# Performance work log

Hardware: AMD Instinct MI355X
Metric: run time of the kernel (lower is better)

Reference implementation:

```python
import jax, jax.numpy as jnp
import numpy as np

B, S, E, H = 2, 2048, 1024, 16
D = E // H  # head_dim = 64

def setup_inputs() -> dict:
    key = jax.random.key(0)
    ks = jax.random.split(key, 11)
    s = 1.0 / np.sqrt(E)
    inp = {
        'query': jax.random.normal(ks[0], (B, S, E), jnp.float32),
        'key':   jax.random.normal(ks[1], (B, S, E), jnp.float32),
        'value': jax.random.normal(ks[2], (B, S, E), jnp.float32),
        'Wq': jax.random.uniform(ks[3], (E, E), jnp.float32, -s, s),
        'bq': jax.random.uniform(ks[4], (E,), jnp.float32, -s, s),
        'Wk': jax.random.uniform(ks[5], (E, E), jnp.float32, -s, s),
        'bk': jax.random.uniform(ks[6], (E,), jnp.float32, -s, s),
        'Wv': jax.random.uniform(ks[7], (E, E), jnp.float32, -s, s),
        'bv': jax.random.uniform(ks[8], (E,), jnp.float32, -s, s),
        'Wo': jax.random.uniform(ks[9], (E, E), jnp.float32, -s, s),
        'bo': jax.random.uniform(ks[10], (E,), jnp.float32, -s, s),
    }
    return inp

def reference(query, key, value, Wq, bq, Wk, bk, Wv, bv, Wo, bo):
    # project and split heads: [B,S,E] -> [B,H,S,D]
    def proj(x, W, b):
        y = jnp.einsum('bse,fe->bsf', x, W) + b  # torch Linear: x @ W.T + b
        return y.reshape(B, S, H, D).transpose(0, 2, 1, 3)
    q = proj(query, Wq, bq)
    k = proj(key, Wk, bk)
    v = proj(value, Wv, bv)
    scores = jnp.einsum('bhqd,bhkd->bhqk', q, k) / jnp.sqrt(jnp.float32(D))
    attn = jax.nn.softmax(scores, axis=-1)
    out = jnp.einsum('bhqk,bhkd->bhqd', attn, v)  # [B,H,S,D]
    out = out.transpose(0, 2, 1, 3).reshape(B, S, E)
    return jnp.einsum('bse,fe->bsf', out, Wo) + bo
```

## Files before the change

### kernel.cpp

```cpp
#include <hip/hip_runtime.h>

#define B_ 2
#define S_ 2048
#define E_ 1024
#define H_ 16
#define D_ 64
#define M_ (B_*S_)
#define K_ E_

typedef __attribute__((ext_vector_type(8))) short  short8;
typedef __attribute__((ext_vector_type(4))) float  f32x4;
typedef __attribute__((ext_vector_type(8))) unsigned short u16x8;
typedef __attribute__((ext_vector_type(4))) unsigned short u16x4;
typedef __attribute__((ext_vector_type(4))) unsigned int   u32x4;

#define QSCALE 0.18033688011112042f

#if __has_builtin(__builtin_amdgcn_exp2f)
#define EXP2F(x) __builtin_amdgcn_exp2f(x)
#else
#define EXP2F(x) exp2f(x)
#endif

__device__ __forceinline__ unsigned short f2bf(float f) {
    unsigned u = __float_as_uint(f);
    u += 0x7fffu + ((u >> 16) & 1u);
    return (unsigned short)(u >> 16);
}

__device__ __forceinline__ void gl_lds16(const ushort* g, ushort* l) {
    __builtin_amdgcn_global_load_lds((const __attribute__((address_space(1))) void*)g,
                                     (__attribute__((address_space(3))) void*)l,
                                     16, 0, 0);
}

#define FL_SYNC(N) do {                                                   \
    asm volatile("s_waitcnt vmcnt(" #N ")" ::: "memory");                 \
    __builtin_amdgcn_s_barrier();                                         \
    asm volatile("" ::: "memory");                                        \
} while (0)

#define WAITL0_BAR() do {                                                 \
    asm volatile("s_waitcnt lgkmcnt(0)" ::: "memory");                    \
    __builtin_amdgcn_s_barrier();                                         \
    asm volatile("" ::: "memory");                                        \
} while (0)

__global__ __launch_bounds__(256)
void cvt_all(const float* __restrict__ q, const float* __restrict__ k,
             const float* __restrict__ v, const float* __restrict__ wq,
             const float* __restrict__ wk, const float* __restrict__ wv,
             const float* __restrict__ wo, ushort* __restrict__ dst)
{
    const int bid = blockIdx.x;
    const float* src;
    size_t dof;
    int local;
    if (bid < 6144) {
        const int t = bid >> 11;
        src = (t == 0) ? q : (t == 1) ? k : v;
        dof = (size_t)t * 4194304u;
        local = bid & 2047;
    } else {
        const int r = bid - 6144;
        const int t = r >> 9;
        src = (t == 0) ? wq : (t == 1) ? wk : (t == 2) ? wv : wo;
        dof = 12582912u + (size_t)t * 1048576u;
        local = r & 511;
    }
    const size_t idx = (size_t)local * 2048 + threadIdx.x * 8;
    const float4 a = *(const float4*)(src + idx);
    const float4 b = *(const float4*)(src + idx + 4);
    u16x8 o;
    o[0] = f2bf(a.x); o[1] = f2bf(a.y); o[2] = f2bf(a.z); o[3] = f2bf(a.w);
    o[4] = f2bf(b.x); o[5] = f2bf(b.y); o[6] = f2bf(b.z); o[7] = f2bf(b.w);
    *(u16x8*)(dst + dof + idx) = o;
}

template<int SWAP>
__device__ __forceinline__ void qkv_core(const ushort* __restrict__ X,
                                         const ushort* __restrict__ W,
                                         int m0, int n0,
                                         f32x4 acc[8][4], ushort* sh)
{
    const int tid  = threadIdx.x;
    const int lane = tid & 63;
    const int w    = tid >> 6;
    const int wm   = w & 1;
    const int wn   = w >> 1;
    const int l15  = lane & 15, quad = lane >> 4;

    const int srow = lane >> 3, schunk = lane & 7;
    const int scol = (schunk ^ srow) * 8;
    const ushort* pa[4]; const ushort* pb[4]; int loff[4];
    #pragma unroll
    for (int i = 0; i < 4; ++i) {
        const int row = (w * 4 + i) * 8 + srow;
        pa[i] = X + (size_t)(m0 + row) * K_ + scol;
        pb[i] = W + (size_t)(n0 + row) * K_ + scol;
        loff[i] = (w * 4 + i) * 512 + lane * 8;
    }

    const f32x4 zero = {0.f, 0.f, 0.f, 0.f};
    #pragma unroll
    for (int mt = 0; mt < 8; ++mt)
        #pragma unroll
        for (int nt = 0; nt < 4; ++nt) acc[mt][nt] = zero;

    #pragma unroll
    for (int i = 0; i < 4; ++i) {
        gl_lds16(pa[i],      sh + loff[i]);
        gl_lds16(pb[i],      sh + 16384 + loff[i]);
    }
    #pragma unroll
    for (int i = 0; i < 4; ++i) {
        gl_lds16(pa[i] + 64, sh + 32768 + loff[i]);
        gl_lds16(pb[i] + 64, sh + 32768 + 16384 + loff[i]);
    }

    const int arow = wm * 128 + l15;
    const int brow = wn * 64 + l15;

    for (int t = 0; t < 16; ++t) {
        ushort* curA = sh + (t & 1) * 32768;
        ushort* curB = curA + 16384;

        if (t < 15) { FL_SYNC(8); } else { FL_SYNC(0); }

        __builtin_amdgcn_s_setprio(1);
        #pragma unroll
        for (int kc = 0; kc < 2; ++kc) {
            short8 bf[4];
            #pragma unroll
            for (int nt = 0; nt < 4; ++nt) {
                const int r = brow + nt * 16;
                bf[nt] = *(const short8*)(curB + r * 64 + (((kc * 4 + quad) ^ (r & 7)) * 8));
            }
            #pragma unroll
            for (int mt = 0; mt < 8; ++mt) {
                const int r = arow + mt * 16;
                const short8 af = *(const short8*)(curA + r * 64 + (((kc * 4 + quad) ^ (r & 7)) * 8));
                #pragma unroll
                for (int nt = 0; nt < 4; ++nt) {
                    if (SWAP)
                        acc[mt][nt] = __builtin_amdgcn_mfma_f32_16x16x32_bf16(bf[nt], af, acc[mt][nt], 0, 0, 0);
                    else
                        acc[mt][nt] = __builtin_amdgcn_mfma_f32_16x16x32_bf16(af, bf[nt], acc[mt][nt], 0, 0, 0);
                }
            }
        }
        __builtin_amdgcn_s_setprio(0);

        if (t + 2 < 16) {
            WAITL0_BAR();
            const int k0 = (t + 2) * 64;
            #pragma unroll
            for (int i = 0; i < 4; ++i) {
                gl_lds16(pa[i] + k0, curA + loff[i]);
                gl_lds16(pb[i] + k0, curB + loff[i]);
            }
        }
    }
}

__global__ __launch_bounds__(512, 2)
void gemm_qkv(const ushort* __restrict__ Xq, const ushort* __restrict__ Xk,
              const ushort* __restrict__ Xv, const ushort* __restrict__ Wq,
              const ushort* __restrict__ Wk, const ushort* __restrict__ Wv,
              const float* __restrict__ bq, const float* __restrict__ bk,
              const float* __restrict__ bv, ushort* __restrict__ Qh,
              ushort* __restrict__ Kh, ushort* __restrict__ Vt)
{
    __shared__ ushort sh[65536];
    const int z = blockIdx.z;
    const ushort* X = (z == 0) ? Xq : (z == 1) ? Xk : Xv;
    const ushort* W = (z == 0) ? Wq : (z == 1) ? Wk : Wv;
    const float* bias = (z == 0) ? bq : (z == 1) ? bk : bv;
    ushort* dst = (z == 0) ? Qh : (z == 1) ? Kh : Vt;

    const int m0 = blockIdx.y * 256, n0 = blockIdx.x * 256;
    f32x4 acc[8][4];
    const int lane = threadIdx.x & 63, w = threadIdx.x >> 6;
    const int wm = w & 1, wn = w >> 1;
    const int l15 = lane & 15, quad = lane >> 4;

    if (z < 2) {
        qkv_core<1>(X, W, m0, n0, acc, sh);
        const float qsc = (z == 0) ? QSCALE : 1.0f;
        #pragma unroll
        for (int nt = 0; nt < 4; ++nt) {
            const int nb = n0 + wn * 64 + nt * 16 + quad * 4;
            const int h = nb >> 6, d0 = nb & 63;
            const float4 b4 = *(const float4*)(bias + nb);
            const float bb4[4] = {b4.x, b4.y, b4.z, b4.w};
            #pragma unroll
            for (int mt = 0; mt < 8; ++mt) {
                const int tok = m0 + wm * 128 + mt * 16 + l15;
                const int b = tok >> 11, s = tok & (S_ - 1);
                u16x4 pk;
                #pragma unroll
                for (int r = 0; r < 4; ++r)
                    pk[r] = f2bf((acc[mt][nt][r] + bb4[r]) * qsc);
                *(u16x4*)&dst[(((size_t)(b * H_ + h) * S_) + s) * D_ + d0] = pk;
            }
        }
    } else {
        qkv_core<0>(X, W, m0, n0, acc, sh);
        float bias4[4];
        #pragma unroll
        for (int nt = 0; nt < 4; ++nt)
            bias4[nt] = bias[n0 + wn * 64 + nt * 16 + l15];
        #pragma unroll
        for (int mt = 0; mt < 8; ++mt) {
            const int mrow0 = m0 + wm * 128 + mt * 16 + (quad * 4);
            const int b = mrow0 >> 11;
            const int s0 = mrow0 & (S_ - 1);
            #pragma unroll
            for (int nt = 0; nt < 4; ++nt) {
                const int n = n0 + wn * 64 + nt * 16 + l15;
                const int h = n >> 6, d = n & 63;
                u16x4 pk;
                #pragma unroll
                for (int r = 0; r < 4; ++r) pk[r] = f2bf(acc[mt][nt][r] + bias4[nt]);
                *(u16x4*)&Vt[(((size_t)(b * H_ + h) * D_) + d) * S_ + s0] = pk;
            }
        }
    }
}

__global__ __launch_bounds__(256)
void gemm_out(const ushort* __restrict__ X, const ushort* __restrict__ W,
              const float* __restrict__ bias, float* __restrict__ out)
{
    __shared__ ushort Ast[128 * 32];
    __shared__ ushort Bst[64 * 32];
    const int m0 = blockIdx.y * 128, n0 = blockIdx.x * 64;
    const int tid = threadIdx.x, lane = tid & 63, w = tid >> 6;
    const int wm = w & 1, wn = w >> 1;
    const int l15 = lane & 15, quad = lane >> 4;
    const int r0 = tid >> 2, c8 = (tid & 3) * 8;
    const int kb = quad * 8;

    const f32x4 zero = {0.f, 0.f, 0.f, 0.f};
    f32x4 acc[4][2];
    #pragma unroll
    for (int mt = 0; mt < 4; ++mt)
        #pragma unroll
        for (int nt = 0; nt < 2; ++nt) acc[mt][nt] = zero;

    for (int k0 = 0; k0 < K_; k0 += 32) {
        __syncthreads();
        const ushort* ga = X + (size_t)(m0 + r0) * K_ + k0 + c8;
        gl_lds16(ga, Ast + tid * 8);
        gl_lds16(ga + (size_t)64 * K_, Ast + 2048 + tid * 8);
        const ushort* gb = W + (size_t)(n0 + r0) * K_ + k0 + c8;
        gl_lds16(gb, Bst + tid * 8);
        __syncthreads();

        short8 af[4], bf[2];
        #pragma unroll
        for (int mt = 0; mt < 4; ++mt)
            af[mt] = *(const short8*)(Ast + (wm * 64 + mt * 16 + l15) * 32 + kb);
        #pragma unroll
        for (int nt = 0; nt < 2; ++nt)
            bf[nt] = *(const short8*)(Bst + (wn * 32 + nt * 16 + l15) * 32 + kb);
        #pragma unroll
        for (int mt = 0; mt < 4; ++mt)
            #pragma unroll
            for (int nt = 0; nt < 2; ++nt)
                acc[mt][nt] = __builtin_amdgcn_mfma_f32_16x16x32_bf16(af[mt], bf[nt], acc[mt][nt], 0, 0, 0);
    }

    float bias2[2];
    #pragma unroll
    for (int nt = 0; nt < 2; ++nt)
        bias2[nt] = bias[n0 + wn * 32 + nt * 16 + l15];

    #pragma unroll
    for (int mt = 0; mt < 4; ++mt) {
        const int mrow0 = m0 + wm * 64 + mt * 16 + quad * 4;
        #pragma unroll
        for (int nt = 0; nt < 2; ++nt) {
            const int n = n0 + wn * 32 + nt * 16 + l15;
            #pragma unroll
            for (int r = 0; r < 4; ++r)
                out[(size_t)(mrow0 + r) * E_ + n] = acc[mt][nt][r] + bias2[nt];
        }
    }
}

#define NTILE (S_ / 64)
#define QBLK 128

__device__ __forceinline__ void flash_stage(const ushort* __restrict__ Kg,
                                            const ushort* __restrict__ Vg,
                                            size_t qk_off, size_t vt_off,
                                            ushort* sh, int j,
                                            int row0, int gcol0, int row1, int gcol1,
                                            int chunk0, int chunk1, int lane)
{
    ushort* sb = sh + 8192 + (j & 1) * 8192;
    const int j0n = j * 64;
    gl_lds16(Kg + qk_off + (size_t)(j0n + row0) * D_ + gcol0 * 8, sb + chunk0 * 512 + lane * 8);
    gl_lds16(Vg + vt_off + (size_t)row0 * S_ + j0n + gcol0 * 8, sb + 4096 + chunk0 * 512 + lane * 8);
    gl_lds16(Kg + qk_off + (size_t)(j0n + row1) * D_ + gcol1 * 8, sb + chunk1 * 512 + lane * 8);
    gl_lds16(Vg + vt_off + (size_t)row1 * S_ + j0n + gcol1 * 8, sb + 4096 + chunk1 * 512 + lane * 8);
}

__global__ __launch_bounds__(256, 2)
void flash_mfma(const ushort* __restrict__ Qg, const ushort* __restrict__ Kg,
                const ushort* __restrict__ Vg, ushort* __restrict__ AO)
{
    __shared__ ushort sh[24576];
    ushort* Qs = sh;

    const int tid = threadIdx.x, lane = tid & 63, w = tid >> 6;
    const int l15 = lane & 15, quad = lane >> 4;
    const int q0 = blockIdx.x * QBLK, h = blockIdx.y, b = blockIdx.z;
    const size_t qk_off = (size_t)(b * H_ + h) * S_ * D_;
    const size_t vt_off = (size_t)(b * H_ + h) * D_ * S_;

    const int chunk0 = w, chunk1 = w + 4;
    const int row0 = chunk0 * 8 + (lane >> 3);
    const int row1 = chunk1 * 8 + (lane >> 3);
    const int gcol0 = (lane & 7) ^ (row0 & 7);
    const int gcol1 = (lane & 7) ^ (row1 & 7);

    #pragma unroll
    for (int i = 0; i < 4; ++i) {
        const int qc = w + i * 4;
        const int qrow = qc * 8 + (lane >> 3);
        const int qg = (lane & 7) ^ (qrow & 7);
        gl_lds16(Qg + qk_off + (size_t)(q0 + qrow) * D_ + qg * 8,
                 Qs + qc * 512 + lane * 8);
    }
    flash_stage(Kg, Vg, qk_off, vt_off, sh, 0, row0, gcol0, row1, gcol1, chunk0, chunk1, lane);
    flash_stage(Kg, Vg, qk_off, vt_off, sh, 1, row0, gcol0, row1, gcol1, chunk0, chunk1, lane);

    FL_SYNC(8);

    f32x4 o[4][4];
    #pragma unroll
    for (int g = 0; g < 4; ++g)
        #pragma unroll
        for (int nt = 0; nt < 4; ++nt) o[g][nt] = {0.f, 0.f, 0.f, 0.f};
    float lsum[4] = {0.f, 0.f, 0.f, 0.f};

    const int qh  = (w >> 1) * 64;
    const int kvb = (w & 1) * 32;
    const int x7  = l15 & 7;
    const int rowA = (kvb + l15) * 64;
    const int rowB = (kvb + 16 + l15) * 64;
    const int gA = ((w & 1) * 4 + (quad >> 1)) ^ x7;
    const int gB = ((w & 1) * 4 + 2 + (quad >> 1)) ^ x7;
    const f32x4 zero = {0.f, 0.f, 0.f, 0.f};

    for (int j = 0; j < NTILE; ++j) {
        const ushort* Kb = sh + 8192 + (j & 1) * 8192;
        const ushort* Vb = Kb + 4096;
        if (j < NTILE - 1) { FL_SYNC(4); } else { FL_SYNC(0); }

        const short8 ka0 = *(const short8*)&Kb[rowA + ((quad ^ x7) * 8)];
        const short8 ka1 = *(const short8*)&Kb[rowA + (((4 + quad) ^ x7) * 8)];
        const short8 ka2 = *(const short8*)&Kb[rowB + ((quad ^ x7) * 8)];
        const short8 ka3 = *(const short8*)&Kb[rowB + (((4 + quad) ^ x7) * 8)];
        uint2 vvA[4], vvB[4];
        #pragma unroll
        for (int nt = 0; nt < 4; ++nt) {
            vvA[nt] = *(const uint2*)&Vb[(nt * 16 + l15) * 64 + gA * 8 + (quad & 1) * 4];
            vvB[nt] = *(const uint2*)&Vb[(nt * 16 + l15) * 64 + gB * 8 + (quad & 1) * 4];
        }

        uint2 paLo[4], paHi[4];
        #pragma unroll
        for (int g = 0; g < 4; ++g) {
            const int qr = (qh + g * 16 + l15) * 64;
            const short8 qg0 = *(const short8*)&Qs[qr + ((quad ^ x7) * 8)];
            const short8 qg1 = *(const short8*)&Qs[qr + (((4 + quad) ^ x7) * 8)];
            f32x4 t = __builtin_amdgcn_mfma_f32_16x16x32_bf16(ka0, qg0, zero, 0, 0, 0);
            t = __builtin_amdgcn_mfma_f32_16x16x32_bf16(ka1, qg1, t, 0, 0, 0);
            f32x4 u = __builtin_amdgcn_mfma_f32_16x16x32_bf16(ka2, qg0, zero, 0, 0, 0);
            u = __builtin_amdgcn_mfma_f32_16x16x32_bf16(ka3, qg1, u, 0, 0, 0);
            {
                const float p0 = EXP2F(t[0]), p1 = EXP2F(t[1]);
                const float p2 = EXP2F(t[2]), p3 = EXP2F(t[3]);
                lsum[g] += (p0 + p1) + (p2 + p3);
                const unsigned a0 = __float_as_uint(p0) + 0x8000u;
                const unsigned a1 = __float_as_uint(p1) + 0x8000u;
                const unsigned a2 = __float_as_uint(p2) + 0x8000u;
                const unsigned a3 = __float_as_uint(p3) + 0x8000u;
                paLo[g].x = (a1 & 0xffff0000u) | (a0 >> 16);
                paLo[g].y = (a3 & 0xffff0000u) | (a2 >> 16);
            }
            {
                const float p0 = EXP2F(u[0]), p1 = EXP2F(u[1]);
                const float p2 = EXP2F(u[2]), p3 = EXP2F(u[3]);
                lsum[g] += (p0 + p1) + (p2 + p3);
                const unsigned a0 = __float_as_uint(p0) + 0x8000u;
                const unsigned a1 = __float_as_uint(p1) + 0x8000u;
                const unsigned a2 = __float_as_uint(p2) + 0x8000u;
                const unsigned a3 = __float_as_uint(p3) + 0x8000u;
                paHi[g].x = (a1 & 0xffff0000u) | (a0 >> 16);
                paHi[g].y = (a3 & 0xffff0000u) | (a2 >> 16);
            }
        }

        short8 pa8[4];
        #pragma unroll
        for (int g = 0; g < 4; ++g) {
            u32x4 pk;
            pk[0] = paLo[g].x; pk[1] = paLo[g].y;
            pk[2] = paHi[g].x; pk[3] = paHi[g].y;
            pa8[g] = __builtin_bit_cast(short8, pk);
        }
        #pragma unroll
        for (int nt = 0; nt < 4; ++nt) {
            u32x4 vk;
            vk[0] = vvA[nt].x; vk[1] = vvA[nt].y;
            vk[2] = vvB[nt].x; vk[3] = vvB[nt].y;
            const short8 vb8 = __builtin_bit_cast(short8, vk);
            #pragma unroll
            for (int g = 0; g < 4; ++g)
                o[g][nt] = __builtin_amdgcn_mfma_f32_16x16x32_bf16(pa8[g], vb8, o[g][nt], 0, 0, 0);
        }

        if (j < NTILE - 2) {
            WAITL0_BAR();
            flash_stage(Kg, Vg, qk_off, vt_off, sh, j + 2,
                        row0, gcol0, row1, gcol1, chunk0, chunk1, lane);
        }
    }

    #pragma unroll
    for (int g = 0; g < 4; ++g) {
        lsum[g] += __shfl_xor(lsum[g], 16);
        lsum[g] += __shfl_xor(lsum[g], 32);
    }
    __syncthreads();
    float* fb = (float*)sh;
    if (w & 1) {
        #pragma unroll
        for (int g = 0; g < 4; ++g) {
            #pragma unroll
            for (int nt = 0; nt < 4; ++nt)
                #pragma unroll
                for (int r = 0; r < 4; ++r)
                    fb[(w >> 1) * 4096 + g * 1024 + (nt * 4 + r) * 64 + lane] = o[g][nt][r];
            if (quad == 0) fb[8192 + (w >> 1) * 64 + g * 16 + l15] = lsum[g];
        }
    }
    __syncthreads();
    if (!(w & 1)) {
        #pragma unroll
        for (int g = 0; g < 4; ++g) {
            #pragma unroll
            for (int nt = 0; nt < 4; ++nt)
                #pragma unroll
                for (int r = 0; r < 4; ++r)
                    o[g][nt][r] += fb[(w >> 1) * 4096 + g * 1024 + (nt * 4 + r) * 64 + lane];
            lsum[g] += fb[8192 + (w >> 1) * 64 + g * 16 + l15];
        }
        #pragma unroll
        for (int g = 0; g < 4; ++g) {
            const float inv = 1.0f / lsum[g];
            float invr[4];
            #pragma unroll
            for (int r = 0; r < 4; ++r)
                invr[r] = __shfl(inv, (lane & 0x30) | (quad * 4 + r));
            #pragma unroll
            for (int nt = 0; nt < 4; ++nt) {
                const int e = h * 64 + nt * 16 + l15;
                #pragma unroll
                for (int r = 0; r < 4; ++r) {
                    const int s = q0 + qh + g * 16 + quad * 4 + r;
                    AO[(size_t)(b * S_ + s) * E_ + e] = f2bf(o[g][nt][r] * invr[r]);
                }
            }
        }
    }
}

extern "C" void kernel_launch(void* const* d_in, const int* in_sizes, int n_in,
                              void* d_out, int out_size, void* d_ws, size_t ws_size,
                              hipStream_t stream) {
    const float* query = (const float*)d_in[0];
    const float* key   = (const float*)d_in[1];
    const float* value = (const float*)d_in[2];
    const float* Wq = (const float*)d_in[3];
    const float* bq = (const float*)d_in[4];
    const float* Wk = (const float*)d_in[5];
    const float* bk = (const float*)d_in[6];
    const float* Wv = (const float*)d_in[7];
    const float* bv = (const float*)d_in[8];
    const float* Wo = (const float*)d_in[9];
    const float* bo = (const float*)d_in[10];
    float* out = (float*)d_out;

    ushort* ws = (ushort*)d_ws;
    ushort* Xq  = ws;
    ushort* Xk  = ws + 4194304u;
    ushort* Xv  = ws + 8388608u;
    ushort* Wqb = ws + 12582912u;
    ushort* Wkb = ws + 13631488u;
    ushort* Wvb = ws + 14680064u;
    ushort* Wob = ws + 15728640u;
    ushort* Qh  = ws + 16777216u;
    ushort* Kh  = ws + 20971520u;
    ushort* Vt  = ws + 25165824u;
    ushort* AO  = ws + 29360128u;

    cvt_all<<<8192, 256, 0, stream>>>(query, key, value, Wq, Wk, Wv, Wo, ws);
    gemm_qkv<<<dim3(4, 16, 3), 512, 0, stream>>>(Xq, Xk, Xv, Wqb, Wkb, Wvb,
                                                 bq, bk, bv, Qh, Kh, Vt);
    flash_mfma<<<dim3(S_ / QBLK, H_, B_), 256, 0, stream>>>(Qh, Kh, Vt, AO);
    gemm_out<<<dim3(16, 32), 256, 0, stream>>>(AO, Wob, bo, out);
}
```

Measured before the change: 225.6 us.

## Load V straight from global into registers and pipeline K-only LDS staging

The flash-attention loop no longer stages V tiles through LDS. Each lane loads its V^T fragments directly from global memory into registers one tile ahead, while only K goes through double-buffered LDS via global_load_lds, which roughly shrinks LDS use from 48KB to 33KB. The loop is unrolled by two with explicit register double buffering and rewritten vmcnt waits, and the manual bf16 packing is replaced by v_cvt_pk_bf16_f32. The risks are extra VGPR pressure, uncoalesced 8-byte global loads for V, and fragile waitcnt accounting.

```diff
diff --git a/kernel.cpp b/kernel.cpp
--- a/kernel.cpp
+++ b/kernel.cpp
@@ -26,6 +26,12 @@
     unsigned u = __float_as_uint(f);
     u += 0x7fffu + ((u >> 16) & 1u);
     return (unsigned short)(u >> 16);
+}
+
+__device__ __forceinline__ unsigned cvtpk(float a, float b) {
+    unsigned r;
+    asm("v_cvt_pk_bf16_f32 %0, %1, %2" : "=v"(r) : "v"(a), "v"(b));
+    return r;
 }
 
 __device__ __forceinline__ void gl_lds16(const ushort* g, ushort* l) {
@@ -292,26 +298,84 @@
 #define NTILE (S_ / 64)
 #define QBLK 128
 
-__device__ __forceinline__ void flash_stage(const ushort* __restrict__ Kg,
-                                            const ushort* __restrict__ Vg,
-                                            size_t qk_off, size_t vt_off,
-                                            ushort* sh, int j,
-                                            int row0, int gcol0, int row1, int gcol1,
-                                            int chunk0, int chunk1, int lane)
-{
-    ushort* sb = sh + 8192 + (j & 1) * 8192;
+__device__ __forceinline__ void flash_stageK(const ushort* __restrict__ Kg,
+                                             size_t qk_off, ushort* sh, int j,
+                                             int row0, int gcol0, int row1, int gcol1,
+                                             int chunk0, int chunk1, int lane)
+{
+    ushort* sb = sh + 8192 + (j & 1) * 4096;
     const int j0n = j * 64;
     gl_lds16(Kg + qk_off + (size_t)(j0n + row0) * D_ + gcol0 * 8, sb + chunk0 * 512 + lane * 8);
-    gl_lds16(Vg + vt_off + (size_t)row0 * S_ + j0n + gcol0 * 8, sb + 4096 + chunk0 * 512 + lane * 8);
     gl_lds16(Kg + qk_off + (size_t)(j0n + row1) * D_ + gcol1 * 8, sb + chunk1 * 512 + lane * 8);
-    gl_lds16(Vg + vt_off + (size_t)row1 * S_ + j0n + gcol1 * 8, sb + 4096 + chunk1 * 512 + lane * 8);
+}
+
+__device__ __forceinline__ void flash_ldK(const ushort* Kslot, int kvb, int l15, int quad,
+                                          short8* ka)
+{
+    const int x7 = l15 & 7;
+    const int rowA = (kvb + l15) * 64, rowB = (kvb + 16 + l15) * 64;
+    ka[0] = *(const short8*)&Kslot[rowA + ((quad ^ x7) * 8)];
+    ka[1] = *(const short8*)&Kslot[rowA + (((4 + quad) ^ x7) * 8)];
+    ka[2] = *(const short8*)&Kslot[rowB + ((quad ^ x7) * 8)];
+    ka[3] = *(const short8*)&Kslot[rowB + (((4 + quad) ^ x7) * 8)];
+}
+
+__device__ __forceinline__ void flash_ldV(const ushort* vb0, int joff,
+                                          uint2* vvA, uint2* vvB)
+{
+    #pragma unroll
+    for (int nt = 0; nt < 4; ++nt) {
+        vvA[nt] = *(const uint2*)(vb0 + (size_t)nt * 16 * S_ + joff);
+        vvB[nt] = *(const uint2*)(vb0 + (size_t)nt * 16 * S_ + joff + 16);
+    }
+}
+
+__device__ __forceinline__ void flash_qkpv(const short8* ka, const ushort* Qs,
+                                           int qh, int l15, int quad,
+                                           const uint2* vvA, const uint2* vvB,
+                                           float* lsum, f32x4 o[4][4])
+{
+    const int x7 = l15 & 7;
+    const f32x4 zero = {0.f, 0.f, 0.f, 0.f};
+    short8 pa8[4];
+    #pragma unroll
+    for (int g = 0; g < 4; ++g) {
+        const int qr = (qh + g * 16 + l15) * 64;
+        const short8 qg0 = *(const short8*)&Qs[qr + ((quad ^ x7) * 8)];
+        const short8 qg1 = *(const short8*)&Qs[qr + (((4 + quad) ^ x7) * 8)];
+        f32x4 t = __builtin_amdgcn_mfma_f32_16x16x32_bf16(ka[0], qg0, zero, 0, 0, 0);
+        t = __builtin_amdgcn_mfma_f32_16x16x32_bf16(ka[1], qg1, t, 0, 0, 0);
+        f32x4 u = __builtin_amdgcn_mfma_f32_16x16x32_bf16(ka[2], qg0, zero, 0, 0, 0);
+        u = __builtin_amdgcn_mfma_f32_16x16x32_bf16(ka[3], qg1, u, 0, 0, 0);
+        const float p0 = EXP2F(t[0]), p1 = EXP2F(t[1]);
+        const float p2 = EXP2F(t[2]), p3 = EXP2F(t[3]);
+        const float r0 = EXP2F(u[0]), r1 = EXP2F(u[1]);
+        const float r2 = EXP2F(u[2]), r3 = EXP2F(u[3]);
+        lsum[g] += ((p0 + p1) + (p2 + p3)) + ((r0 + r1) + (r2 + r3));
+        u32x4 pk;
+        pk[0] = cvtpk(p0, p1);
+        pk[1] = cvtpk(p2, p3);
+        pk[2] = cvtpk(r0, r1);
+        pk[3] = cvtpk(r2, r3);
+        pa8[g] = __builtin_bit_cast(short8, pk);
+    }
+    #pragma unroll
+    for (int nt = 0; nt < 4; ++nt) {
+        u32x4 vk;
+        vk[0] = vvA[nt].x; vk[1] = vvA[nt].y;
+        vk[2] = vvB[nt].x; vk[3] = vvB[nt].y;
+        const short8 vb8 = __builtin_bit_cast(short8, vk);
+        #pragma unroll
+        for (int g = 0; g < 4; ++g)
+            o[g][nt] = __builtin_amdgcn_mfma_f32_16x16x32_bf16(pa8[g], vb8, o[g][nt], 0, 0, 0);
+    }
 }
 
 __global__ __launch_bounds__(256, 2)
 void flash_mfma(const ushort* __restrict__ Qg, const ushort* __restrict__ Kg,
                 const ushort* __restrict__ Vg, ushort* __restrict__ AO)
 {
-    __shared__ ushort sh[24576];
+    __shared__ ushort sh[16640];
     ushort* Qs = sh;
 
     const int tid = threadIdx.x, lane = tid & 63, w = tid >> 6;
@@ -325,6 +389,11 @@
     const int row1 = chunk1 * 8 + (lane >> 3);
     const int gcol0 = (lane & 7) ^ (row0 & 7);
     const int gcol1 = (lane & 7) ^ (row1 & 7);
+
+    const int qh  = (w >> 1) * 64;
+    const int kvb = (w & 1) * 32;
+    const int cA = ((w & 1) * 4 + (quad >> 1)) * 8 + (quad & 1) * 4;
+    const ushort* vb0 = Vg + vt_off + (size_t)l15 * S_ + cA;
 
     #pragma unroll
     for (int i = 0; i < 4; ++i) {
@@ -334,10 +403,10 @@
         gl_lds16(Qg + qk_off + (size_t)(q0 + qrow) * D_ + qg * 8,
                  Qs + qc * 512 + lane * 8);
     }
-    flash_stage(Kg, Vg, qk_off, vt_off, sh, 0, row0, gcol0, row1, gcol1, chunk0, chunk1, lane);
-    flash_stage(Kg, Vg, qk_off, vt_off, sh, 1, row0, gcol0, row1, gcol1, chunk0, chunk1, lane);
-
-    FL_SYNC(8);
+    flash_stageK(Kg, qk_off, sh, 0, row0, gcol0, row1, gcol1, chunk0, chunk1, lane);
+    flash_stageK(Kg, qk_off, sh, 1, row0, gcol0, row1, gcol1, chunk0, chunk1, lane);
+    uint2 vA0[4], vB0[4], vA1[4], vB1[4];
+    flash_ldV(vb0, 0, vA0, vB0);
 
     f32x4 o[4][4];
     #pragma unroll
@@ -346,90 +415,33 @@
         for (int nt = 0; nt < 4; ++nt) o[g][nt] = {0.f, 0.f, 0.f, 0.f};
     float lsum[4] = {0.f, 0.f, 0.f, 0.f};
 
-    const int qh  = (w >> 1) * 64;
-    const int kvb = (w & 1) * 32;
-    const int x7  = l15 & 7;
-    const int rowA = (kvb + l15) * 64;
-    const int rowB = (kvb + 16 + l15) * 64;
-    const int gA = ((w & 1) * 4 + (quad >> 1)) ^ x7;
-    const int gB = ((w & 1) * 4 + 2 + (quad >> 1)) ^ x7;
-    const f32x4 zero = {0.f, 0.f, 0.f, 0.f};
-
-    for (int j = 0; j < NTILE; ++j) {
-        const ushort* Kb = sh + 8192 + (j & 1) * 8192;
-        const ushort* Vb = Kb + 4096;
-        if (j < NTILE - 1) { FL_SYNC(4); } else { FL_SYNC(0); }
-
-        const short8 ka0 = *(const short8*)&Kb[rowA + ((quad ^ x7) * 8)];
-        const short8 ka1 = *(const short8*)&Kb[rowA + (((4 + quad) ^ x7) * 8)];
-        const short8 ka2 = *(const short8*)&Kb[rowB + ((quad ^ x7) * 8)];
-        const short8 ka3 = *(const short8*)&Kb[rowB + (((4 + quad) ^ x7) * 8)];
-        uint2 vvA[4], vvB[4];
-        #pragma unroll
-        for (int nt = 0; nt < 4; ++nt) {
-            vvA[nt] = *(const uint2*)&Vb[(nt * 16 + l15) * 64 + gA * 8 + (quad & 1) * 4];
-            vvB[nt] = *(const uint2*)&Vb[(nt * 16 + l15) * 64 + gB * 8 + (quad & 1) * 4];
-        }
-
-        uint2 paLo[4], paHi[4];
-        #pragma unroll
-        for (int g = 0; g < 4; ++g) {
-            const int qr = (qh + g * 16 + l15) * 64;
-            const short8 qg0 = *(const short8*)&Qs[qr + ((quad ^ x7) * 8)];
-            const short8 qg1 = *(const short8*)&Qs[qr + (((4 + quad) ^ x7) * 8)];
-            f32x4 t = __builtin_amdgcn_mfma_f32_16x16x32_bf16(ka0, qg0, zero, 0, 0, 0);
-            t = __builtin_amdgcn_mfma_f32_16x16x32_bf16(ka1, qg1, t, 0, 0, 0);
-            f32x4 u = __builtin_amdgcn_mfma_f32_16x16x32_bf16(ka2, qg0, zero, 0, 0, 0);
-            u = __builtin_amdgcn_mfma_f32_16x16x32_bf16(ka3, qg1, u, 0, 0, 0);
-            {
-                const float p0 = EXP2F(t[0]), p1 = EXP2F(t[1]);
-                const float p2 = EXP2F(t[2]), p3 = EXP2F(t[3]);
-                lsum[g] += (p0 + p1) + (p2 + p3);
-                const unsigned a0 = __float_as_uint(p0) + 0x8000u;
-                const unsigned a1 = __float_as_uint(p1) + 0x8000u;
-                const unsigned a2 = __float_as_uint(p2) + 0x8000u;
-                const unsigned a3 = __float_as_uint(p3) + 0x8000u;
-                paLo[g].x = (a1 & 0xffff0000u) | (a0 >> 16);
-                paLo[g].y = (a3 & 0xffff0000u) | (a2 >> 16);
-            }
-            {
-                const float p0 = EXP2F(u[0]), p1 = EXP2F(u[1]);
-                const float p2 = EXP2F(u[2]), p3 = EXP2F(u[3]);
-                lsum[g] += (p0 + p1) + (p2 + p3);
-                const unsigned a0 = __float_as_uint(p0) + 0x8000u;
-                const unsigned a1 = __float_as_uint(p1) + 0x8000u;
-                const unsigned a2 = __float_as_uint(p2) + 0x8000u;
-                const unsigned a3 = __float_as_uint(p3) + 0x8000u;
-                paHi[g].x = (a1 & 0xffff0000u) | (a0 >> 16);
-                paHi[g].y = (a3 & 0xffff0000u) | (a2 >> 16);
-            }
-        }
-
-        short8 pa8[4];
-        #pragma unroll
-        for (int g = 0; g < 4; ++g) {
-            u32x4 pk;
-            pk[0] = paLo[g].x; pk[1] = paLo[g].y;
-            pk[2] = paHi[g].x; pk[3] = paHi[g].y;
-            pa8[g] = __builtin_bit_cast(short8, pk);
-        }
-        #pragma unroll
-        for (int nt = 0; nt < 4; ++nt) {
-            u32x4 vk;
-            vk[0] = vvA[nt].x; vk[1] = vvA[nt].y;
-            vk[2] = vvB[nt].x; vk[3] = vvB[nt].y;
-            const short8 vb8 = __builtin_bit_cast(short8, vk);
-            #pragma unroll
-            for (int g = 0; g < 4; ++g)
-                o[g][nt] = __builtin_amdgcn_mfma_f32_16x16x32_bf16(pa8[g], vb8, o[g][nt], 0, 0, 0);
-        }
-
-        if (j < NTILE - 2) {
-            WAITL0_BAR();
-            flash_stage(Kg, Vg, qk_off, vt_off, sh, j + 2,
-                        row0, gcol0, row1, gcol1, chunk0, chunk1, lane);
-        }
-    }
+    const ushort* slot0 = sh + 8192;
+    const ushort* slot1 = sh + 12288;
+    short8 ka[4];
+
+    for (int p = 0; p < 15; ++p) {
+        const int jA = 2 * p;
+        FL_SYNC(10);
+        flash_ldK(slot0, kvb, l15, quad, ka);
+        WAITL0_BAR();
+        flash_stageK(Kg, qk_off, sh, jA + 2, row0, gcol0, row1, gcol1, chunk0, chunk1, lane);
+        flash_ldV(vb0, (jA + 1) * 64, vA1, vB1);
+        flash_qkpv(ka, Qs, qh, l15, quad, vA0, vB0, lsum, o);
+        FL_SYNC(10);
+        flash_ldK(slot1, kvb, l15, quad, ka);
+        WAITL0_BAR();
+        flash_stageK(Kg, qk_off, sh, jA + 3, row0, gcol0, row1, gcol1, chunk0, chunk1, lane);
+        flash_ldV(vb0, (jA + 2) * 64, vA0, vB0);
+        flash_qkpv(ka, Qs, qh, l15, quad, vA1, vB1, lsum, o);
+    }
+
+    FL_SYNC(10);
+    flash_ldK(slot0, kvb, l15, quad, ka);
+    flash_ldV(vb0, 31 * 64, vA1, vB1);
+    flash_qkpv(ka, Qs, qh, l15, quad, vA0, vB0, lsum, o);
+    FL_SYNC(8);
+    flash_ldK(slot1, kvb, l15, quad, ka);
+    flash_qkpv(ka, Qs, qh, l15, quad, vA1, vB1, lsum, o);
 
     #pragma unroll
     for (int g = 0; g < 4; ++g) {
```

Result: slower. 244.0 us (+8.1%).
